# Performance work log

Hardware: AMD Instinct MI355X
Metric: run time of the kernel (lower is better)

The kernel has to match this reference:

```python
import jax, jax.numpy as jnp
import numpy as np

H = 4      # SSM / attn heads (d_model/headdim = 256/64)
WIN = 4    # attention window over bands


def _ln(x, g, b):
    m = jnp.mean(x, -1, keepdims=True)
    v = jnp.mean((x - m) ** 2, -1, keepdims=True)
    return (x - m) * jax.lax.rsqrt(v + 1e-5) * g + b


def setup_inputs() -> dict:
    key = jax.random.key(0)
    ks = jax.random.split(key, 24)
    def rn(i, shape, s=0.05):
        return jax.random.normal(ks[i], shape, jnp.float32) * s
    B, T, K, D = 2, 256, 8, 256
    return {
        "z": rn(0, (B, T, K, D), 1.0),
        "ln1_g": jnp.ones((D,), jnp.float32), "ln1_b": jnp.zeros((D,), jnp.float32),
        "Wx": rn(1, (D, D)), "conv_w": rn(2, (D, 4), 0.3), "Wz": rn(3, (D, D)),
        "Wb": rn(4, (D, H * 128)), "Wc": rn(5, (D, H * 128)), "Wdt": rn(6, (D, H)),
        "dt_bias": rn(7, (H,), 0.5), "A_log": rn(8, (H,), 0.5), "theta": rn(9, (H,), 1.0),
        "D_skip": rn(10, (H,), 1.0), "mimo_U": rn(11, (H, H), 0.5), "mimo_V": rn(12, (H, H), 0.5),
        "Wout": rn(13, (D, D)),
        "ln2_g": jnp.ones((D,), jnp.float32), "ln2_b": jnp.zeros((D,), jnp.float32),
        "attn_in_w": rn(14, (3 * D, D)), "attn_in_b": rn(15, (3 * D,), 0.02),
        "attn_out_w": rn(16, (D, D)), "attn_out_b": jnp.zeros((D,), jnp.float32),
        "ln3_g": jnp.ones((D,), jnp.float32), "ln3_b": jnp.zeros((D,), jnp.float32),
        "Wg": rn(17, (D, 4 * D)), "Wu": rn(18, (D, 4 * D)), "Wd": rn(19, (4 * D, D)),
    }


def _forward(z, ln1_g, ln1_b, Wx, conv_w, Wz, Wb, Wc, Wdt, dt_bias, A_log, theta,
             D_skip, mimo_U, mimo_V, Wout, ln2_g, ln2_b, attn_in_w, attn_in_b,
             attn_out_w, attn_out_b, ln3_g, ln3_b, Wg, Wu, Wd):
    B, T, K, D = z.shape
    P = D // H
    N = Wb.shape[1] // H
    # ---------- (a) intra-band Mamba3 (complex MIMO selective scan) ----------
    u = _ln(z, ln1_g, ln1_b)
    u = jnp.transpose(u, (0, 2, 1, 3)).reshape(B * K, T, D)   # [BK,T,D]
    x = u @ Wx
    # causal depthwise conv1d, kernel 4
    xp = jnp.pad(x, ((0, 0), (3, 0), (0, 0)))
    x = sum(xp[:, k:k + T, :] * conv_w[:, k] for k in range(4))
    x = jax.nn.silu(x)
    xh = x.reshape(B * K, T, H, P)
    Bm = (u @ Wb).reshape(B * K, T, H, N)
    Cm = (u @ Wc).reshape(B * K, T, H, N)
    Mmix = mimo_U @ mimo_V.T                                  # rank-r cross-head coupling
    Bm = jnp.einsum('hg,btgn->bthn', Mmix, Bm)
    dt = jax.nn.softplus(u @ Wdt + dt_bias)                   # [BK,T,H]
    A = -jnp.exp(A_log)                                       # stable real decay
    mag = jnp.exp(dt * A)
    ph = dt * theta                                           # harmonic rotation
    ar, ai = mag * jnp.cos(ph), mag * jnp.sin(ph)
    xs = tuple(jnp.moveaxis(t, 1, 0) for t in (xh, Bm, Cm, dt, ar, ai))
    h0 = jnp.zeros((B * K, H, N, P), x.dtype)

    def step(carry, s):
        h_re, h_im = carry
        xt, bt, ct, dtt, art, ait = s
        dBx = (dtt[:, :, None, None] * bt[:, :, :, None]) * xt[:, :, None, :]
        nr = art[:, :, None, None] * h_re - ait[:, :, None, None] * h_im + dBx
        ni = art[:, :, None, None] * h_im + ait[:, :, None, None] * h_re
        return (nr, ni), jnp.einsum('bhn,bhnp->bhp', ct, nr)   # Re(C . h)

    _, ys = jax.lax.scan(step, (h0, h0), xs)                  # ys: [T,BK,H,P]
    y = jnp.moveaxis(ys, 0, 1) + D_skip[None, None, :, None] * xh
    y = y.reshape(B * K, T, D) * jax.nn.silu(u @ Wz)
    y = y @ Wout
    z = z + jnp.transpose(y.reshape(B, K, T, D), (0, 2, 1, 3))
    # ---------- (b) inter-band windowed attention ----------
    zn = _ln(z, ln2_g, ln2_b).reshape(B * T, K, D)
    qkv = zn @ attn_in_w.T + attn_in_b
    q, k_, v = jnp.split(qkv, 3, axis=-1)
    hd = D // H
    def hs(t):
        return t.reshape(B * T, K // WIN, WIN, H, hd).transpose(0, 1, 3, 2, 4)
    q, k_, v = hs(q), hs(k_), hs(v)
    s = jnp.einsum('mwhqd,mwhkd->mwhqk', q, k_) * jnp.float32(1.0 / np.sqrt(hd))
    a = jax.nn.softmax(s, axis=-1)
    o = jnp.einsum('mwhqk,mwhkd->mwhqd', a, v).transpose(0, 1, 3, 2, 4).reshape(B * T, K, D)
    z = z + (o @ attn_out_w.T + attn_out_b).reshape(B, T, K, D)
    # ---------- (c) SwiGLU FFN ----------
    zf = _ln(z, ln3_g, ln3_b)
    z = z + (jax.nn.silu(zf @ Wg) * (zf @ Wu)) @ Wd
    return z


def reference(z, ln1_g, ln1_b, Wx, conv_w, Wz, Wb, Wc, Wdt, dt_bias, A_log, theta,
              D_skip, mimo_U, mimo_V, Wout, ln2_g, ln2_b, attn_in_w, attn_in_b,
              attn_out_w, attn_out_b, ln3_g, ln3_b, Wg, Wu, Wd):
    return _forward(z, ln1_g, ln1_b, Wx, conv_w, Wz, Wb, Wc, Wdt, dt_bias, A_log,
                    theta, D_skip, mimo_U, mimo_V, Wout, ln2_g, ln2_b, attn_in_w,
                    attn_in_b, attn_out_w, attn_out_b, ln3_g, ln3_b, Wg, Wu, Wd)
```

## Files before the change

kernel.cpp:

```cpp
#include <hip/hip_runtime.h>
#include <hip/hip_bf16.h>
#include <math.h>

typedef __hip_bfloat16 bf16;
typedef __attribute__((ext_vector_type(8))) short s16x8;
typedef __attribute__((ext_vector_type(4))) float f32x4;

__device__ __forceinline__ float siluf(float x) { return x / (1.f + __expf(-x)); }
__device__ __forceinline__ float bits2f(unsigned short u) {
    union { float f; unsigned i; } v; v.i = ((unsigned)u) << 16; return v.f;
}
__device__ __forceinline__ unsigned short f2bits(float f) {
    return (unsigned short)__bfloat16_as_ushort(__float2bfloat16(f));
}

#define KFL 1024
#define OFF_UB   (768*KFL)
#define OFF_DTV  (1280*KFL)
#define OFF_BMB  (1344*KFL)
#define OFF_CMB  (2368*KFL)
#define OFF_ZGB  (3392*KFL)
#define OFF_XB   (3904*KFL)
#define OFF_X2T  (4928*KFL)
#define OFF_P    (5440*KFL)
// ... 66 lines not shown
                for (int j = 0; j < 4; j++) s += U[h * 4 + j] * V[g * 4 + j];
                mm[g] = s;
            }
            #pragma unroll
            for (int i = 0; i < 16; i++) {
                int idx = tid + i * 256;
                int kk = idx >> 6, nn = idx & 63;
                const float* row = src + (size_t)(k0 + kk) * 512 + scol + nn;
                lds[kk * 65 + nn] = mm[0] * row[0] + mm[1] * row[128]
                                  + mm[2] * row[256] + mm[3] * row[384];
            }
        } else {
            #pragma unroll
            for (int i = 0; i < 16; i++) {
                int idx = tid + i * 256;
                int kk = idx >> 6, nn = idx & 63;
                lds[kk * 65 + nn] = src[(size_t)(k0 + kk) * srcN + sc0 + nn];
            }
        }
        __syncthreads();
        #pragma unroll
        for (int i = 0; i < 16; i++) {
            int idx = tid + i * 256;
            int nn = idx >> 6, kk = idx & 63;
            wout[dstoff + (size_t)(n0 + nn) * dstK + k0 + kk] = f2bits(lds[kk * 65 + nn]);
        }
        return;
    }
    int r = blk - 368;
    float* lds = smem;
    float* dts = smem + 4;
    int t = r & 255, bk = r >> 8;
    int b_ = bk >> 3, k = bk & 7;
    int srcr = ((b_ * 256 + t) * 8 + k) * 256;
    int d = tid;
    float x = z[srcr + d];
    float v = x;
    #pragma unroll
    for (int off = 32; off; off >>= 1) v += __shfl_xor(v, off, 64);
    if ((d & 63) == 0) lds[d >> 6] = v;
    __syncthreads();
    float mean = (lds[0] + lds[1] + lds[2] + lds[3]) * (1.f / 256.f);
    __syncthreads();
    float c = x - mean;
    v = c * c;
    #pragma unroll
    for (int off = 32; off; off >>= 1) v += __shfl_xor(v, off, 64);
    if ((d & 63) == 0) lds[d >> 6] = v;
    __syncthreads();
    float var = (lds[0] + lds[1] + lds[2] + lds[3]) * (1.f / 256.f);
    float uval = c * rsqrtf(var + 1e-5f) * g1[d] + b1[d];
    u[r * 256 + d] = f2bits(uval);
    float4 wv = *(const float4*)(Wdt + d * 4);
    float q0 = uval * wv.x, q1 = uval * wv.y, q2 = uval * wv.z, q3 = uval * wv.w;
    #pragma unroll
    for (int off = 32; off; off >>= 1) {
        q0 += __shfl_xor(q0, off, 64);
        q1 += __shfl_xor(q1, off, 64);
        q2 += __shfl_xor(q2, off, 64);
        q3 += __shfl_xor(q3, off, 64);
    }
    if ((d & 63) == 0) {
        int w = d >> 6;
        dts[w * 4 + 0] = q0; dts[w * 4 + 1] = q1;
        dts[w * 4 + 2] = q2; dts[w * 4 + 3] = q3;
    }
    __syncthreads();
    if (d == 0) {
        float dv[4];
        #pragma unroll
        for (int h = 0; h < 4; h++) {
            float xx = dts[h] + dts[4 + h] + dts[8 + h] + dts[12 + h] + dt_bias[h];
            dv[h] = (xx > 20.f) ? xx : log1pf(__expf(xx));
        }
        dtv4[r] = make_float4(dv[0], dv[1], dv[2], dv[3]);
    }
}

__global__ __launch_bounds__(256) void gemm_bczx(
    const unsigned short* __restrict__ A, const unsigned short* __restrict__ Bt,
    unsigned short* __restrict__ bmb, unsigned short* __restrict__ cmb,
    unsigned short* __restrict__ zgb, unsigned short* __restrict__ xb)
{
    __shared__ __align__(16) unsigned short As[128 * 72];
    __shared__ __align__(16) unsigned short Bs[128 * 72];
    const int K = 256;
    int tid = threadIdx.x;
    int n0 = blockIdx.x * 128, m0 = blockIdx.y * 128;
    int w = tid >> 6, l = tid & 63;
    int mwave = (w >> 1) * 64, nwave = (w & 1) * 64;
    f32x4 acc[4][4] = {};
    int srow = tid >> 3, sc = (tid & 7) * 8;
    const unsigned short* Ap = A + (size_t)(m0 + srow) * K + sc;
    const unsigned short* Bp = Bt + (size_t)(n0 + srow) * K + sc;
    int lq = l & 15, lh = l >> 4;
    uint4 a0 = *(const uint4*)(Ap);
    uint4 a1 = *(const uint4*)(Ap + (size_t)32 * K);
    uint4 a2 = *(const uint4*)(Ap + (size_t)64 * K);
    uint4 a3 = *(const uint4*)(Ap + (size_t)96 * K);
    uint4 b0 = *(const uint4*)(Bp);
    uint4 b1 = *(const uint4*)(Bp + (size_t)32 * K);
    uint4 b2 = *(const uint4*)(Bp + (size_t)64 * K);
    uint4 b3 = *(const uint4*)(Bp + (size_t)96 * K);
    for (int k0 = 0; k0 < K; k0 += 64) {
        if (k0) __syncthreads();
        *(uint4*)&As[srow * 72 + sc] = a0;
        *(uint4*)&As[(srow + 32) * 72 + sc] = a1;
        *(uint4*)&As[(srow + 64) * 72 + sc] = a2;
        *(uint4*)&As[(srow + 96) * 72 + sc] = a3;
        *(uint4*)&Bs[srow * 72 + sc] = b0;
        *(uint4*)&Bs[(srow + 32) * 72 + sc] = b1;
        *(uint4*)&Bs[(srow + 64) * 72 + sc] = b2;
        *(uint4*)&Bs[(srow + 96) * 72 + sc] = b3;
        __syncthreads();
        if (k0 + 64 < K) {
            a0 = *(const uint4*)(Ap + k0 + 64);
            a1 = *(const uint4*)(Ap + (size_t)32 * K + k0 + 64);
            a2 = *(const uint4*)(Ap + (size_t)64 * K + k0 + 64);
            a3 = *(const uint4*)(Ap + (size_t)96 * K + k0 + 64);
            b0 = *(const uint4*)(Bp + k0 + 64);
            b1 = *(const uint4*)(Bp + (size_t)32 * K + k0 + 64);
            b2 = *(const uint4*)(Bp + (size_t)64 * K + k0 + 64);
            b3 = *(const uint4*)(Bp + (size_t)96 * K + k0 + 64);
        }
        #pragma unroll
        for (int kk = 0; kk < 2; kk++) {
            int kof = kk * 32 + lh * 8;
            s16x8 bfr[4];
            #pragma unroll
            for (int nf = 0; nf < 4; nf++)
                bfr[nf] = *(const s16x8*)&Bs[(nwave + nf * 16 + lq) * 72 + kof];
            #pragma unroll
            for (int mf = 0; mf < 4; mf++) {
                s16x8 af = *(const s16x8*)&As[(mwave + mf * 16 + lq) * 72 + kof];
                #pragma unroll
                for (int nf = 0; nf < 4; nf++)
                    acc[mf][nf] = __builtin_amdgcn_mfma_f32_16x16x32_bf16(af, bfr[nf], acc[mf][nf], 0, 0, 0);
            }
        }
    }
    #pragma unroll
    for (int mf = 0; mf < 4; mf++) {
        #pragma unroll
        for (int nf = 0; nf < 4; nf++) {
            int n = n0 + nwave + nf * 16 + lq;
            #pragma unroll
            for (int r = 0; r < 4; r++) {
                int m = m0 + mwave + mf * 16 + (l >> 4) * 4 + r;
                float v = acc[mf][nf][r];
                if (n < 512)       bmb[(size_t)m * 512 + n] = f2bits(v);
                else if (n < 1024) cmb[(size_t)m * 512 + (n - 512)] = f2bits(v);
                else if (n < 1280) zgb[(size_t)m * 256 + (n - 1024)] = f2bits(siluf(v));
                else               xb[(size_t)m * 256 + (n - 1280)] = f2bits(v);
            }
        }
    }
}

__global__ __launch_bounds__(256) void s_conv_kernel(
    const unsigned short* __restrict__ cmb, const unsigned short* __restrict__ bmb,
    const float4* __restrict__ dtv4, const float* __restrict__ A_log,
    const float* __restrict__ theta, unsigned short* __restrict__ P,
    const unsigned short* __restrict__ xb, const float* __restrict__ cw,
    unsigned short* __restrict__ x2t)
{
    __shared__ __align__(16) char smem[39936];
    int blk = blockIdx.x;
    int tid = threadIdx.x;
    if (blk >= 192) {
        int c = blk - 192;
        int bhid = c >> 2, tt = c & 3;
        int bk = bhid >> 2, h = bhid & 3;
        int t0 = tt * 64;
        float* tile = (float*)smem;
        #pragma unroll
        for (int i = 0; i < 17; i++) {
            int idx = tid + i * 256;
            if (idx < 67 * 64) {
                int tr = idx >> 6, dd = idx & 63;
                int t = t0 - 3 + tr;
                tile[tr * 65 + dd] = (t >= 0)
                    ? bits2f(xb[(size_t)(bk * 256 + t) * 256 + h * 64 + dd]) : 0.f;
            }
        }
        __syncthreads();
        int wv_ = tid >> 6, lt = tid & 63;
        #pragma unroll 4
        for (int pi = 0; pi < 16; pi++) {
            int p = wv_ * 16 + pi;
            float4 wv = *(const float4*)(cw + (h * 64 + p) * 4);
            float acc = tile[lt * 65 + p] * wv.x + tile[(lt + 1) * 65 + p] * wv.y +
                        tile[(lt + 2) * 65 + p] * wv.z + tile[(lt + 3) * 65 + p] * wv.w;
            x2t[(size_t)(bhid * 64 + p) * 256 + t0 + lt] = f2bits(siluf(acc));
        }
        return;
    }
    int map = blk >> 6;
    int bh = blk & 63;
    int bx = (map == 2) ? 1 : 0;
    int by = (map == 0) ? 0 : 1;
    int bk = bh >> 2, h = bh & 3;
    unsigned short* As = (unsigned short*)smem;
    unsigned short* Bs = As + 128 * 72;
    float* mAs = (float*)(smem + 36864);
    float* phs = mAs + 256;
    float* dss = phs + 256;
    int srow = tid >> 3, sc = (tid & 7) * 8;
    const unsigned short* Ap = cmb + (size_t)(bk * 256 + by * 128 + srow) * 512 + h * 128 + sc;
    const unsigned short* Bp = bmb + (size_t)(bk * 256 + bx * 128 + srow) * 512 + h * 128 + sc;
    uint4 a0 = *(const uint4*)(Ap);
    uint4 a1 = *(const uint4*)(Ap + (size_t)32 * 512);
    uint4 a2 = *(const uint4*)(Ap + (size_t)64 * 512);
    uint4 a3 = *(const uint4*)(Ap + (size_t)96 * 512);
    uint4 b0 = *(const uint4*)(Bp);
    uint4 b1 = *(const uint4*)(Bp + (size_t)32 * 512);
    uint4 b2 = *(const uint4*)(Bp + (size_t)64 * 512);
    uint4 b3 = *(const uint4*)(Bp + (size_t)96 * 512);
    {
        float4 dv = dtv4[bk * 256 + tid];
        float dth = (h == 0) ? dv.x : (h == 1) ? dv.y : (h == 2) ? dv.z : dv.w;
        float Ah = -__expf(A_log[h]);
        float th = theta[h];
        dss[tid] = dth;
        mAs[tid] = dth * Ah;
        phs[tid] = dth * th;
        __syncthreads();
        for (int off = 1; off < 256; off <<= 1) {
            float a = 0.f, p = 0.f;
            int use = (tid >= off);
            if (use) { a = mAs[tid - off]; p = phs[tid - off]; }
            __syncthreads();
            if (use) { mAs[tid] += a; phs[tid] += p; }
            __syncthreads();
        }
    }
    int w = tid >> 6, l = tid & 63;
    int mwave = (w >> 1) * 64, nwave = (w & 1) * 64;
    int lq = l & 15, lh = l >> 4;
    unsigned short* Pout = P + (size_t)bh * 65536;
    f32x4 acc[4][4] = {};
    for (int k0 = 0; k0 < 128; k0 += 64) {
        __syncthreads();
        *(uint4*)&As[srow * 72 + sc] = a0;
        *(uint4*)&As[(srow + 32) * 72 + sc] = a1;
        *(uint4*)&As[(srow + 64) * 72 + sc] = a2;
        *(uint4*)&As[(srow + 96) * 72 + sc] = a3;
        *(uint4*)&Bs[srow * 72 + sc] = b0;
        *(uint4*)&Bs[(srow + 32) * 72 + sc] = b1;
        *(uint4*)&Bs[(srow + 64) * 72 + sc] = b2;
        *(uint4*)&Bs[(srow + 96) * 72 + sc] = b3;
        __syncthreads();
        if (k0 + 64 < 128) {
            a0 = *(const uint4*)(Ap + k0 + 64);
            a1 = *(const uint4*)(Ap + (size_t)32 * 512 + k0 + 64);
            a2 = *(const uint4*)(Ap + (size_t)64 * 512 + k0 + 64);
            a3 = *(const uint4*)(Ap + (size_t)96 * 512 + k0 + 64);
            b0 = *(const uint4*)(Bp + k0 + 64);
            b1 = *(const uint4*)(Bp + (size_t)32 * 512 + k0 + 64);
            b2 = *(const uint4*)(Bp + (size_t)64 * 512 + k0 + 64);
            b3 = *(const uint4*)(Bp + (size_t)96 * 512 + k0 + 64);
        }
        #pragma unroll
        for (int kk = 0; kk < 2; kk++) {
            int kof = kk * 32 + lh * 8;
            s16x8 bfr[4];
            #pragma unroll
            for (int nf = 0; nf < 4; nf++)
                bfr[nf] = *(const s16x8*)&Bs[(nwave + nf * 16 + lq) * 72 + kof];
            #pragma unroll
            for (int mf = 0; mf < 4; mf++) {
                s16x8 af = *(const s16x8*)&As[(mwave + mf * 16 + lq) * 72 + kof];
                #pragma unroll
                for (int nf = 0; nf < 4; nf++)
                    acc[mf][nf] = __builtin_amdgcn_mfma_f32_16x16x32_bf16(af, bfr[nf], acc[mf][nf], 0, 0, 0);
            }
        }
    }
    #pragma unroll
    for (int mf = 0; mf < 4; mf++) {
        float tmv[4], tpv[4]; int tg[4];
        #pragma unroll
        for (int r = 0; r < 4; r++) {
            tg[r] = by * 128 + mwave + mf * 16 + lh * 4 + r;
            tmv[r] = mAs[tg[r]];
            tpv[r] = phs[tg[r]];
        }
        #pragma unroll
        for (int nf = 0; nf < 4; nf++) {
            int s = bx * 128 + nwave + nf * 16 + lq;
            float ms = mAs[s];
            float ps = phs[s];
            float ds = dss[s];
            #pragma unroll
            for (int r = 0; r < 4; r++) {
                float wgt = (s <= tg[r])
                    ? __expf(tmv[r] - ms) * __cosf(tpv[r] - ps) * ds : 0.f;
                Pout[tg[r] * 256 + s] = f2bits(acc[mf][nf][r] * wgt);
            }
        }
    }
}

__global__ __launch_bounds__(256) void gemm_y(
    const unsigned short* __restrict__ P, const unsigned short* __restrict__ x2t,
    const unsigned short* __restrict__ zgb, const float* __restrict__ Dsk,
    unsigned short* __restrict__ ygb)
{
    int by = blockIdx.x, bh = blockIdx.y;
    int bk = bh >> 2, h = bh & 3;
    int tid = threadIdx.x;
    int w = tid >> 6, l = tid & 63;
    int mw = (w >> 1) * 32, nw = (w & 1) * 32;
    int lq = l & 15, lh = l >> 4;
    __shared__ __align__(16) unsigned short As[64 * 72];
    __shared__ __align__(16) unsigned short Bs[64 * 72];
    f32x4 acc[2][2] = {};
    int srow = tid >> 3, sc = (tid & 7) * 8;
    const unsigned short* Ap = P + (size_t)bh * 65536 + (size_t)(by * 64 + srow) * 256 + sc;
    const unsigned short* Bp = x2t + (size_t)bh * 16384 + (size_t)srow * 256 + sc;
    int kmax = (by + 1) * 64; if (kmax > 256) kmax = 256;
    uint4 a0 = *(const uint4*)(Ap);
    uint4 a1 = *(const uint4*)(Ap + (size_t)32 * 256);
    uint4 b0 = *(const uint4*)(Bp);
    uint4 b1 = *(const uint4*)(Bp + (size_t)32 * 256);
    for (int k0 = 0; k0 < kmax; k0 += 64) {
        if (k0) __syncthreads();
        *(uint4*)&As[srow * 72 + sc] = a0;
        *(uint4*)&As[(srow + 32) * 72 + sc] = a1;
        *(uint4*)&Bs[srow * 72 + sc] = b0;
        *(uint4*)&Bs[(srow + 32) * 72 + sc] = b1;
        __syncthreads();
        if (k0 + 64 < kmax) {
            a0 = *(const uint4*)(Ap + k0 + 64);
            a1 = *(const uint4*)(Ap + (size_t)32 * 256 + k0 + 64);
            b0 = *(const uint4*)(Bp + k0 + 64);
            b1 = *(const uint4*)(Bp + (size_t)32 * 256 + k0 + 64);
        }
        #pragma unroll
        for (int kk = 0; kk < 2; kk++) {
            int kof = kk * 32 + lh * 8;
            s16x8 bfr[2];
            #pragma unroll
            for (int nf = 0; nf < 2; nf++)
                bfr[nf] = *(const s16x8*)&Bs[(nw + nf * 16 + lq) * 72 + kof];
            #pragma unroll
            for (int mf = 0; mf < 2; mf++) {
                s16x8 af = *(const s16x8*)&As[(mw + mf * 16 + lq) * 72 + kof];
                #pragma unroll
                for (int nf = 0; nf < 2; nf++)
                    acc[mf][nf] = __builtin_amdgcn_mfma_f32_16x16x32_bf16(af, bfr[nf], acc[mf][nf], 0, 0, 0);
            }
        }
    }
    float dsk = Dsk[h];
    #pragma unroll
    for (int mf = 0; mf < 2; mf++) {
        #pragma unroll
        for (int nf = 0; nf < 2; nf++) {
            int p = nw + nf * 16 + lq;
            #pragma unroll
            for (int r = 0; r < 4; r++) {
                int t = by * 64 + mw + mf * 16 + lh * 4 + r;
                float xv = bits2f(x2t[(size_t)bh * 16384 + p * 256 + t]);
                float zg = bits2f(zgb[(size_t)(bk * 256 + t) * 256 + h * 64 + p]);
                ygb[(size_t)(bk * 256 + t) * 256 + h * 64 + p] =
                    f2bits((acc[mf][nf][r] + dsk * xv) * zg);
            }
        }
    }
}

__global__ __launch_bounds__(256) void mid_kernel(
    const unsigned short* __restrict__ ygb, const unsigned short* __restrict__ wts,
    const float* __restrict__ zin,
    const float* __restrict__ g2, const float* __restrict__ b2,
    const float* __restrict__ qbias, const float* __restrict__ obias,
    const float* __restrict__ g3, const float* __restrict__ b3,
    float* __restrict__ z2, unsigned short* __restrict__ zfb)
{
    __shared__ __align__(16) char smem[64512];
    unsigned short* Bs = (unsigned short*)smem;
    unsigned short* As = (unsigned short*)(smem + 36864);
    unsigned short* zn = (unsigned short*)(smem + 39168);
    float* z1s = (float*)(smem + 47616);
    float (*partS)[4] = (float(*)[4])(smem + 64000);
    float (*partQ)[4] = (float(*)[4])(smem + 64256);
    unsigned short* qk = (unsigned short*)smem;

    const int K = 256;
    int tid = threadIdx.x;
    int m0 = blockIdx.x * 16;
    int w = tid >> 6, l = tid & 63;
    int nw = w * 64;
    int lq = l & 15, lh = l >> 4;
    int srow = tid >> 3, sc = (tid & 7) * 8;

    {
        int rb = m0 + (srow & 15);
        int irow = ((rb >> 11) * 8 + (rb & 7)) * 256 + ((rb >> 3) & 255);
        const unsigned short* Ap = ygb + (size_t)irow * K + sc;
        const unsigned short* Bp = wts + W_OUT + (size_t)srow * K + sc;
        f32x4 acc[4] = {};
        uint4 a0 = *(const uint4*)(Ap);
        uint4 c0 = *(const uint4*)(Bp);
        uint4 c1 = *(const uint4*)(Bp + (size_t)32 * K);
        uint4 c2 = *(const uint4*)(Bp + (size_t)64 * K);
        uint4 c3 = *(const uint4*)(Bp + (size_t)96 * K);
        uint4 c4 = *(const uint4*)(Bp + (size_t)128 * K);
        uint4 c5 = *(const uint4*)(Bp + (size_t)160 * K);
        uint4 c6 = *(const uint4*)(Bp + (size_t)192 * K);
        uint4 c7 = *(const uint4*)(Bp + (size_t)224 * K);
        for (int k0 = 0; k0 < K; k0 += 64) {
            if (k0) __syncthreads();
            if (tid < 128) *(uint4*)&As[srow * 72 + sc] = a0;
            *(uint4*)&Bs[srow * 72 + sc] = c0;
            *(uint4*)&Bs[(srow + 32) * 72 + sc] = c1;
            *(uint4*)&Bs[(srow + 64) * 72 + sc] = c2;
            *(uint4*)&Bs[(srow + 96) * 72 + sc] = c3;
            *(uint4*)&Bs[(srow + 128) * 72 + sc] = c4;
            *(uint4*)&Bs[(srow + 160) * 72 + sc] = c5;
            *(uint4*)&Bs[(srow + 192) * 72 + sc] = c6;
            *(uint4*)&Bs[(srow + 224) * 72 + sc] = c7;
            __syncthreads();
            if (k0 + 64 < K) {
                a0 = *(const uint4*)(Ap + k0 + 64);
                c0 = *(const uint4*)(Bp + k0 + 64);
                c1 = *(const uint4*)(Bp + (size_t)32 * K + k0 + 64);
                c2 = *(const uint4*)(Bp + (size_t)64 * K + k0 + 64);
                c3 = *(const uint4*)(Bp + (size_t)96 * K + k0 + 64);
                c4 = *(const uint4*)(Bp + (size_t)128 * K + k0 + 64);
                c5 = *(const uint4*)(Bp + (size_t)160 * K + k0 + 64);
                c6 = *(const uint4*)(Bp + (size_t)192 * K + k0 + 64);
                c7 = *(const uint4*)(Bp + (size_t)224 * K + k0 + 64);
            }
            #pragma unroll
            for (int kk = 0; kk < 2; kk++) {
                int kof = kk * 32 + lh * 8;
                s16x8 af = *(const s16x8*)&As[lq * 72 + kof];
                #pragma unroll
                for (int nf = 0; nf < 4; nf++) {
                    s16x8 bf = *(const s16x8*)&Bs[(nw + nf * 16 + lq) * 72 + kof];
                    acc[nf] = __builtin_amdgcn_mfma_f32_16x16x32_bf16(af, bf, acc[nf], 0, 0, 0);
                }
            }
        }
        #pragma unroll
        for (int r = 0; r < 4; r++) {
            int row = lh * 4 + r;
            float s = 0.f, q = 0.f;
            #pragma unroll
// ... 148 lines not shown
        for (int k0 = 0; k0 < K; k0 += 64) {
            __syncthreads();
            *(uint4*)&Bs[srow * 72 + sc] = c0;
            *(uint4*)&Bs[(srow + 32) * 72 + sc] = c1;
            *(uint4*)&Bs[(srow + 64) * 72 + sc] = c2;
            *(uint4*)&Bs[(srow + 96) * 72 + sc] = c3;
            *(uint4*)&Bs[(srow + 128) * 72 + sc] = c4;
            *(uint4*)&Bs[(srow + 160) * 72 + sc] = c5;
            *(uint4*)&Bs[(srow + 192) * 72 + sc] = c6;
            *(uint4*)&Bs[(srow + 224) * 72 + sc] = c7;
            __syncthreads();
            if (k0 + 64 < K) {
                c0 = *(const uint4*)(Bp4 + k0 + 64);
                c1 = *(const uint4*)(Bp4 + (size_t)32 * K + k0 + 64);
                c2 = *(const uint4*)(Bp4 + (size_t)64 * K + k0 + 64);
                c3 = *(const uint4*)(Bp4 + (size_t)96 * K + k0 + 64);
                c4 = *(const uint4*)(Bp4 + (size_t)128 * K + k0 + 64);
                c5 = *(const uint4*)(Bp4 + (size_t)160 * K + k0 + 64);
                c6 = *(const uint4*)(Bp4 + (size_t)192 * K + k0 + 64);
                c7 = *(const uint4*)(Bp4 + (size_t)224 * K + k0 + 64);
            }
            #pragma unroll
            for (int kk = 0; kk < 2; kk++) {
                int kof = kk * 32 + lh * 8;
                s16x8 af = *(const s16x8*)&zn[lq * 264 + k0 + kof];
                #pragma unroll
                for (int nf = 0; nf < 4; nf++) {
                    s16x8 bf = *(const s16x8*)&Bs[(nw + nf * 16 + lq) * 72 + kof];
                    ac4[nf] = __builtin_amdgcn_mfma_f32_16x16x32_bf16(af, bf, ac4[nf], 0, 0, 0);
                }
            }
        }
        float bv[4], gv[4], bbv[4];
        #pragma unroll
        for (int nf = 0; nf < 4; nf++) {
            int n = nw + nf * 16 + lq;
            bv[nf] = obias[n];
            gv[nf] = g3[n];
            bbv[nf] = b3[n];
        }
        #pragma unroll
        for (int r = 0; r < 4; r++) {
            int row = lh * 4 + r;
            float s = 0.f, q = 0.f;
            #pragma unroll
            for (int nf = 0; nf < 4; nf++) {
                float v = ac4[nf][r] + bv[nf] + z1s[row * 256 + nw + nf * 16 + lq];
                ac4[nf][r] = v;
                s += v; q += v * v;
            }
            #pragma unroll
            for (int off = 1; off < 16; off <<= 1) {
                s += __shfl_xor(s, off, 64);
                q += __shfl_xor(q, off, 64);
            }
            if (lq == 0) { partS[row][w] = s; partQ[row][w] = q; }
        }
        __syncthreads();
        #pragma unroll
        for (int r = 0; r < 4; r++) {
            int row = lh * 4 + r;
            float sum = partS[row][0] + partS[row][1] + partS[row][2] + partS[row][3];
            float sq  = partQ[row][0] + partQ[row][1] + partQ[row][2] + partQ[row][3];
            float mean = sum * (1.f / 256.f);
            float var = sq * (1.f / 256.f) - mean * mean;
            float rstd = rsqrtf(var + 1e-5f);
            size_t ro = (size_t)(m0 + row) * 256;
            #pragma unroll
            for (int nf = 0; nf < 4; nf++) {
                int n = nw + nf * 16 + lq;
                float v = ac4[nf][r];
                z2[ro + n] = v;
                zfb[ro + n] = f2bits((v - mean) * rstd * gv[nf] + bbv[nf]);
            }
        }
    }
}

__global__ __launch_bounds__(256) void gemm_gu2(
    const unsigned short* __restrict__ A, const unsigned short* __restrict__ Wgu,
    unsigned short* __restrict__ gg)
{
    const int K = 256;
    __shared__ __align__(16) unsigned short As[128 * 72];
    __shared__ __align__(16) unsigned short Bgs[64 * 72];
    __shared__ __align__(16) unsigned short Bus[64 * 72];
    int tid = threadIdx.x;
    int n0 = blockIdx.x * 64, m0 = blockIdx.y * 128;
    int w = tid >> 6, l = tid & 63;
    int mwave = (w >> 1) * 64, nwave = (w & 1) * 32;
    int lq = l & 15, lh = l >> 4;
    f32x4 ag[4][2] = {}, au[4][2] = {};
    int srow = tid >> 3, sc = (tid & 7) * 8;
    const unsigned short* Ap = A + (size_t)(m0 + srow) * K + sc;
    const unsigned short* Bgp = Wgu + (size_t)(n0 + srow) * K + sc;
    const unsigned short* Bup = Wgu + (size_t)(1024 + n0 + srow) * K + sc;
    uint4 a0 = *(const uint4*)(Ap);
    uint4 a1 = *(const uint4*)(Ap + (size_t)32 * K);
    uint4 a2 = *(const uint4*)(Ap + (size_t)64 * K);
    uint4 a3 = *(const uint4*)(Ap + (size_t)96 * K);
    uint4 bg0 = *(const uint4*)(Bgp);
    uint4 bg1 = *(const uint4*)(Bgp + (size_t)32 * K);
    uint4 bu0 = *(const uint4*)(Bup);
    uint4 bu1 = *(const uint4*)(Bup + (size_t)32 * K);
    for (int k0 = 0; k0 < K; k0 += 64) {
        if (k0) __syncthreads();
        *(uint4*)&As[srow * 72 + sc] = a0;
        *(uint4*)&As[(srow + 32) * 72 + sc] = a1;
        *(uint4*)&As[(srow + 64) * 72 + sc] = a2;
        *(uint4*)&As[(srow + 96) * 72 + sc] = a3;
        *(uint4*)&Bgs[srow * 72 + sc] = bg0;
        *(uint4*)&Bgs[(srow + 32) * 72 + sc] = bg1;
        *(uint4*)&Bus[srow * 72 + sc] = bu0;
        *(uint4*)&Bus[(srow + 32) * 72 + sc] = bu1;
        __syncthreads();
        if (k0 + 64 < K) {
            a0 = *(const uint4*)(Ap + k0 + 64);
            a1 = *(const uint4*)(Ap + (size_t)32 * K + k0 + 64);
            a2 = *(const uint4*)(Ap + (size_t)64 * K + k0 + 64);
            a3 = *(const uint4*)(Ap + (size_t)96 * K + k0 + 64);
            bg0 = *(const uint4*)(Bgp + k0 + 64);
            bg1 = *(const uint4*)(Bgp + (size_t)32 * K + k0 + 64);
            bu0 = *(const uint4*)(Bup + k0 + 64);
            bu1 = *(const uint4*)(Bup + (size_t)32 * K + k0 + 64);
        }
        #pragma unroll
        for (int kk = 0; kk < 2; kk++) {
            int kof = kk * 32 + lh * 8;
            s16x8 bgr[2], bur[2];
            #pragma unroll
            for (int nf = 0; nf < 2; nf++) {
                bgr[nf] = *(const s16x8*)&Bgs[(nwave + nf * 16 + lq) * 72 + kof];
                bur[nf] = *(const s16x8*)&Bus[(nwave + nf * 16 + lq) * 72 + kof];
            }
            #pragma unroll
            for (int mf = 0; mf < 4; mf++) {
                s16x8 af = *(const s16x8*)&As[(mwave + mf * 16 + lq) * 72 + kof];
                #pragma unroll
                for (int nf = 0; nf < 2; nf++) {
                    ag[mf][nf] = __builtin_amdgcn_mfma_f32_16x16x32_bf16(af, bgr[nf], ag[mf][nf], 0, 0, 0);
                    au[mf][nf] = __builtin_amdgcn_mfma_f32_16x16x32_bf16(af, bur[nf], au[mf][nf], 0, 0, 0);
                }
            }
        }
    }
    #pragma unroll
    for (int mf = 0; mf < 4; mf++) {
        #pragma unroll
        for (int nf = 0; nf < 2; nf++) {
            int n = n0 + nwave + nf * 16 + lq;
            #pragma unroll
            for (int r = 0; r < 4; r++) {
                int m = m0 + mwave + mf * 16 + lh * 4 + r;
                gg[(size_t)m * 1024 + n] = f2bits(siluf(ag[mf][nf][r]) * au[mf][nf][r]);
            }
        }
    }
}

__global__ __launch_bounds__(256) void gemm_d2(
    const unsigned short* __restrict__ gg, const unsigned short* __restrict__ Bt,
    const float* __restrict__ resid, float* __restrict__ out)
{
    __shared__ __align__(16) unsigned short As[64 * 72];
    __shared__ __align__(16) unsigned short Bs[64 * 72];
    const int K = 1024, N = 256;
    int tid = threadIdx.x;
    int n0 = blockIdx.x * 64, m0 = blockIdx.y * 64;
    int w = tid >> 6, l = tid & 63;
    int mw = (w >> 1) * 32, nw = (w & 1) * 32;
    f32x4 acc[2][2] = {};
    int srow = tid >> 3, sc = (tid & 7) * 8;
    const unsigned short* Ap = gg + (size_t)(m0 + srow) * K + sc;
    const unsigned short* Bp = Bt + (size_t)(n0 + srow) * K + sc;
    int lq = l & 15, lh = l >> 4;
    uint4 a0 = *(const uint4*)(Ap);
    uint4 a1 = *(const uint4*)(Ap + (size_t)32 * K);
    uint4 b0 = *(const uint4*)(Bp);
    uint4 b1 = *(const uint4*)(Bp + (size_t)32 * K);
    for (int k0 = 0; k0 < K; k0 += 64) {
        if (k0) __syncthreads();
        *(uint4*)&As[srow * 72 + sc] = a0;
        *(uint4*)&As[(srow + 32) * 72 + sc] = a1;
        *(uint4*)&Bs[srow * 72 + sc] = b0;
        *(uint4*)&Bs[(srow + 32) * 72 + sc] = b1;
        __syncthreads();
        if (k0 + 64 < K) {
            a0 = *(const uint4*)(Ap + k0 + 64);
            a1 = *(const uint4*)(Ap + (size_t)32 * K + k0 + 64);
            b0 = *(const uint4*)(Bp + k0 + 64);
            b1 = *(const uint4*)(Bp + (size_t)32 * K + k0 + 64);
        }
        #pragma unroll
        for (int kk = 0; kk < 2; kk++) {
            int kof = kk * 32 + lh * 8;
            s16x8 bfr[2];
            #pragma unroll
            for (int nf = 0; nf < 2; nf++)
                bfr[nf] = *(const s16x8*)&Bs[(nw + nf * 16 + lq) * 72 + kof];
            #pragma unroll
            for (int mf = 0; mf < 2; mf++) {
                s16x8 af = *(const s16x8*)&As[(mw + mf * 16 + lq) * 72 + kof];
                #pragma unroll
                for (int nf = 0; nf < 2; nf++)
                    acc[mf][nf] = __builtin_amdgcn_mfma_f32_16x16x32_bf16(af, bfr[nf], acc[mf][nf], 0, 0, 0);
            }
        }
    }
    #pragma unroll
    for (int mf = 0; mf < 2; mf++) {
        #pragma unroll
        for (int nf = 0; nf < 2; nf++) {
            int n = n0 + nw + nf * 16 + lq;
            #pragma unroll
            for (int r = 0; r < 4; r++) {
                int m = m0 + mw + mf * 16 + lh * 4 + r;
                out[(size_t)m * N + n] = acc[mf][nf][r] + resid[(size_t)m * N + n];
            }
        }
    }
}

extern "C" void kernel_launch(void* const* d_in, const int* in_sizes, int n_in,
                              void* d_out, int out_size, void* d_ws, size_t ws_size,
                              hipStream_t stream)
{
    const float* z         = (const float*)d_in[0];
    const float* ln1_g     = (const float*)d_in[1];
    const float* ln1_b     = (const float*)d_in[2];
    const float* Wx        = (const float*)d_in[3];
    const float* conv_w    = (const float*)d_in[4];
    const float* Wz        = (const float*)d_in[5];
    const float* Wb        = (const float*)d_in[6];
    const float* Wc        = (const float*)d_in[7];
    const float* Wdt       = (const float*)d_in[8];
    const float* dt_bias   = (const float*)d_in[9];
    const float* A_log     = (const float*)d_in[10];
    const float* theta     = (const float*)d_in[11];
    const float* D_skip    = (const float*)d_in[12];
    const float* mimo_U    = (const float*)d_in[13];
    const float* mimo_V    = (const float*)d_in[14];
    const float* Wout      = (const float*)d_in[15];
    const float* ln2_g     = (const float*)d_in[16];
    const float* ln2_b     = (const float*)d_in[17];
    const float* attn_in_w = (const float*)d_in[18];
    const float* attn_in_b = (const float*)d_in[19];
    const float* attn_out_w= (const float*)d_in[20];
    const float* attn_out_b= (const float*)d_in[21];
    const float* ln3_g     = (const float*)d_in[22];
    const float* ln3_b     = (const float*)d_in[23];
    const float* Wg        = (const float*)d_in[24];
    const float* Wu        = (const float*)d_in[25];
    const float* Wd        = (const float*)d_in[26];

    float* W = (float*)d_ws;
    unsigned short* wts = (unsigned short*)W;
    unsigned short* ub  = (unsigned short*)(W + OFF_UB);
    float4* dtv4        = (float4*)(W + OFF_DTV);
    unsigned short* bmb = (unsigned short*)(W + OFF_BMB);
    unsigned short* cmb = (unsigned short*)(W + OFF_CMB);
    unsigned short* zgb = (unsigned short*)(W + OFF_ZGB);
    unsigned short* xb  = (unsigned short*)(W + OFF_XB);
    unsigned short* x2t = (unsigned short*)(W + OFF_X2T);
    unsigned short* pbuf= (unsigned short*)(W + OFF_P);
    unsigned short* ygb = (unsigned short*)(W + OFF_YGB);
    float* z2           = W + OFF_Z2;
    unsigned short* zfb = (unsigned short*)(W + OFF_ZFB);
    unsigned short* gg  = (unsigned short*)(W + OFF_GG);

    prep_ln1_kernel<<<4464, 256, 0, stream>>>(
        Wx, Wb, Wc, Wz, Wout, attn_in_w, attn_out_w, Wg, Wu, Wd, mimo_U, mimo_V,
        wts, z, ln1_g, ln1_b, Wdt, dt_bias, ub, dtv4);
    gemm_bczx<<<dim3(12, 32), 256, 0, stream>>>(ub, wts + W_BCZX, bmb, cmb, zgb, xb);
    s_conv_kernel<<<448, 256, 0, stream>>>(cmb, bmb, dtv4, A_log, theta, pbuf,
                                           xb, conv_w, x2t);
    gemm_y<<<dim3(4, 64), 256, 0, stream>>>(pbuf, x2t, zgb, D_skip, ygb);
    mid_kernel<<<256, 256, 0, stream>>>(ygb, wts, z, ln2_g, ln2_b,
                                        attn_in_b, attn_out_b, ln3_g, ln3_b,
                                        z2, zfb);
    gemm_gu2<<<dim3(16, 32), 256, 0, stream>>>(zfb, wts + W_GU, gg);
    gemm_d2<<<dim3(4, 64), 256, 0, stream>>>(gg, wts + W_D, z2, (float*)d_out);
}
```

Before: 198.6 us.

## Halve GEMM tiles to double grid sizes and use wave-shuffle prefix scan

Halves the M or N tile size in the four GEMM kernels (bczx, y, gu2, d2) and doubles their grid dimensions, so more workgroups are spread across the many compute units. The intent is to fill the GPU better on these small problems. The cost is less data reuse per tile and more redundant loads of the shared operand. Separately, the 256-element prefix scan in s_conv is replaced: a shared-memory Hillis-Steele loop with many barriers becomes a per-wave __shfl_up scan plus a cross-wave offset step. This removes most __syncthreads calls. In gemm_y the causal k-limit is recomputed for 32-row tiles.

New measurement: 198.7 us. Within noise of the previous version (+0.1%).

```diff
diff --git a/kernel.cpp b/kernel.cpp
--- a/kernel.cpp
+++ b/kernel.cpp
@@ -172,22 +172,20 @@
     unsigned short* __restrict__ bmb, unsigned short* __restrict__ cmb,
     unsigned short* __restrict__ zgb, unsigned short* __restrict__ xb)
 {
-    __shared__ __align__(16) unsigned short As[128 * 72];
+    __shared__ __align__(16) unsigned short As[64 * 72];
     __shared__ __align__(16) unsigned short Bs[128 * 72];
     const int K = 256;
     int tid = threadIdx.x;
-    int n0 = blockIdx.x * 128, m0 = blockIdx.y * 128;
+    int n0 = blockIdx.x * 128, m0 = blockIdx.y * 64;
     int w = tid >> 6, l = tid & 63;
-    int mwave = (w >> 1) * 64, nwave = (w & 1) * 64;
-    f32x4 acc[4][4] = {};
+    int mwave = (w >> 1) * 32, nwave = (w & 1) * 64;
+    f32x4 acc[2][4] = {};
     int srow = tid >> 3, sc = (tid & 7) * 8;
     const unsigned short* Ap = A + (size_t)(m0 + srow) * K + sc;
     const unsigned short* Bp = Bt + (size_t)(n0 + srow) * K + sc;
     int lq = l & 15, lh = l >> 4;
     uint4 a0 = *(const uint4*)(Ap);
     uint4 a1 = *(const uint4*)(Ap + (size_t)32 * K);
-    uint4 a2 = *(const uint4*)(Ap + (size_t)64 * K);
-    uint4 a3 = *(const uint4*)(Ap + (size_t)96 * K);
     uint4 b0 = *(const uint4*)(Bp);
     uint4 b1 = *(const uint4*)(Bp + (size_t)32 * K);
     uint4 b2 = *(const uint4*)(Bp + (size_t)64 * K);
@@ -196,8 +194,6 @@
         if (k0) __syncthreads();
         *(uint4*)&As[srow * 72 + sc] = a0;
         *(uint4*)&As[(srow + 32) * 72 + sc] = a1;
-        *(uint4*)&As[(srow + 64) * 72 + sc] = a2;
-        *(uint4*)&As[(srow + 96) * 72 + sc] = a3;
         *(uint4*)&Bs[srow * 72 + sc] = b0;
         *(uint4*)&Bs[(srow + 32) * 72 + sc] = b1;
         *(uint4*)&Bs[(srow + 64) * 72 + sc] = b2;
@@ -206,8 +202,6 @@
         if (k0 + 64 < K) {
             a0 = *(const uint4*)(Ap + k0 + 64);
             a1 = *(const uint4*)(Ap + (size_t)32 * K + k0 + 64);
-            a2 = *(const uint4*)(Ap + (size_t)64 * K + k0 + 64);
-            a3 = *(const uint4*)(Ap + (size_t)96 * K + k0 + 64);
             b0 = *(const uint4*)(Bp + k0 + 64);
             b1 = *(const uint4*)(Bp + (size_t)32 * K + k0 + 64);
             b2 = *(const uint4*)(Bp + (size_t)64 * K + k0 + 64);
@@ -221,7 +215,7 @@
             for (int nf = 0; nf < 4; nf++)
                 bfr[nf] = *(const s16x8*)&Bs[(nwave + nf * 16 + lq) * 72 + kof];
             #pragma unroll
-            for (int mf = 0; mf < 4; mf++) {
+            for (int mf = 0; mf < 2; mf++) {
                 s16x8 af = *(const s16x8*)&As[(mwave + mf * 16 + lq) * 72 + kof];
                 #pragma unroll
                 for (int nf = 0; nf < 4; nf++)
@@ -230,13 +224,13 @@
         }
     }
     #pragma unroll
-    for (int mf = 0; mf < 4; mf++) {
+    for (int mf = 0; mf < 2; mf++) {
         #pragma unroll
         for (int nf = 0; nf < 4; nf++) {
             int n = n0 + nwave + nf * 16 + lq;
             #pragma unroll
             for (int r = 0; r < 4; r++) {
-                int m = m0 + mwave + mf * 16 + (l >> 4) * 4 + r;
+                int m = m0 + mwave + mf * 16 + lh * 4 + r;
                 float v = acc[mf][nf][r];
                 if (n < 512)       bmb[(size_t)m * 512 + n] = f2bits(v);
                 else if (n < 1024) cmb[(size_t)m * 512 + (n - 512)] = f2bits(v);
@@ -311,18 +305,25 @@
         float dth = (h == 0) ? dv.x : (h == 1) ? dv.y : (h == 2) ? dv.z : dv.w;
         float Ah = -__expf(A_log[h]);
         float th = theta[h];
+        float a = dth * Ah, p = dth * th;
         dss[tid] = dth;
-        mAs[tid] = dth * Ah;
-        phs[tid] = dth * th;
-        __syncthreads();
-        for (int off = 1; off < 256; off <<= 1) {
-            float a = 0.f, p = 0.f;
-            int use = (tid >= off);
-            if (use) { a = mAs[tid - off]; p = phs[tid - off]; }
-            __syncthreads();
-            if (use) { mAs[tid] += a; phs[tid] += p; }
-            __syncthreads();
-        }
+        int lane = tid & 63, wv = tid >> 6;
+        #pragma unroll
+        for (int off = 1; off < 64; off <<= 1) {
+            float ta = __shfl_up(a, off, 64);
+            float tp = __shfl_up(p, off, 64);
+            if (lane >= off) { a += ta; p += tp; }
+        }
+        if (lane == 63) { mAs[wv] = a; phs[wv] = p; }
+        __syncthreads();
+        float offA = 0.f, offP = 0.f;
+        #pragma unroll
+        for (int j = 0; j < 3; j++)
+            if (j < wv) { offA += mAs[j]; offP += phs[j]; }
+        __syncthreads();
+        mAs[tid] = a + offA;
+        phs[tid] = p + offP;
+        __syncthreads();
     }
     int w = tid >> 6, l = tid & 63;
     int mwave = (w >> 1) * 64, nwave = (w & 1) * 64;
@@ -398,64 +399,56 @@
 {
     int by = blockIdx.x, bh = blockIdx.y;
     int bk = bh >> 2, h = bh & 3;
+    int t0 = by * 32;
     int tid = threadIdx.x;
     int w = tid >> 6, l = tid & 63;
-    int mw = (w >> 1) * 32, nw = (w & 1) * 32;
+    int mw = (w >> 1) * 16, nw = (w & 1) * 32;
     int lq = l & 15, lh = l >> 4;
-    __shared__ __align__(16) unsigned short As[64 * 72];
+    __shared__ __align__(16) unsigned short As[32 * 72];
     __shared__ __align__(16) unsigned short Bs[64 * 72];
-    f32x4 acc[2][2] = {};
+    f32x4 acc[2] = {};
     int srow = tid >> 3, sc = (tid & 7) * 8;
-    const unsigned short* Ap = P + (size_t)bh * 65536 + (size_t)(by * 64 + srow) * 256 + sc;
+    const unsigned short* Ap = P + (size_t)bh * 65536 + (size_t)(t0 + srow) * 256 + sc;
     const unsigned short* Bp = x2t + (size_t)bh * 16384 + (size_t)srow * 256 + sc;
-    int kmax = (by + 1) * 64; if (kmax > 256) kmax = 256;
+    int kmax = ((by >> 1) + 1) * 64;
     uint4 a0 = *(const uint4*)(Ap);
-    uint4 a1 = *(const uint4*)(Ap + (size_t)32 * 256);
     uint4 b0 = *(const uint4*)(Bp);
     uint4 b1 = *(const uint4*)(Bp + (size_t)32 * 256);
     for (int k0 = 0; k0 < kmax; k0 += 64) {
         if (k0) __syncthreads();
-        *(uint4*)&As[srow * 72 + sc] = a0;
-        *(uint4*)&As[(srow + 32) * 72 + sc] = a1;
+        if (tid < 256) {
+            *(uint4*)&As[(srow & 31) * 72 + sc] = a0;
+        }
         *(uint4*)&Bs[srow * 72 + sc] = b0;
         *(uint4*)&Bs[(srow + 32) * 72 + sc] = b1;
         __syncthreads();
         if (k0 + 64 < kmax) {
             a0 = *(const uint4*)(Ap + k0 + 64);
-            a1 = *(const uint4*)(Ap + (size_t)32 * 256 + k0 + 64);
             b0 = *(const uint4*)(Bp + k0 + 64);
             b1 = *(const uint4*)(Bp + (size_t)32 * 256 + k0 + 64);
         }
         #pragma unroll
         for (int kk = 0; kk < 2; kk++) {
             int kof = kk * 32 + lh * 8;
-            s16x8 bfr[2];
-            #pragma unroll
-            for (int nf = 0; nf < 2; nf++)
-                bfr[nf] = *(const s16x8*)&Bs[(nw + nf * 16 + lq) * 72 + kof];
-            #pragma unroll
-            for (int mf = 0; mf < 2; mf++) {
-                s16x8 af = *(const s16x8*)&As[(mw + mf * 16 + lq) * 72 + kof];
-                #pragma unroll
-                for (int nf = 0; nf < 2; nf++)
-                    acc[mf][nf] = __builtin_amdgcn_mfma_f32_16x16x32_bf16(af, bfr[nf], acc[mf][nf], 0, 0, 0);
+            s16x8 af = *(const s16x8*)&As[(mw + lq) * 72 + kof];
+            #pragma unroll
+            for (int nf = 0; nf < 2; nf++) {
+                s16x8 bf = *(const s16x8*)&Bs[(nw + nf * 16 + lq) * 72 + kof];
+                acc[nf] = __builtin_amdgcn_mfma_f32_16x16x32_bf16(af, bf, acc[nf], 0, 0, 0);
             }
         }
     }
     float dsk = Dsk[h];
     #pragma unroll
-    for (int mf = 0; mf < 2; mf++) {
-        #pragma unroll
-        for (int nf = 0; nf < 2; nf++) {
-            int p = nw + nf * 16 + lq;
-            #pragma unroll
-            for (int r = 0; r < 4; r++) {
-                int t = by * 64 + mw + mf * 16 + lh * 4 + r;
-                float xv = bits2f(x2t[(size_t)bh * 16384 + p * 256 + t]);
-                float zg = bits2f(zgb[(size_t)(bk * 256 + t) * 256 + h * 64 + p]);
-                ygb[(size_t)(bk * 256 + t) * 256 + h * 64 + p] =
-                    f2bits((acc[mf][nf][r] + dsk * xv) * zg);
-            }
+    for (int nf = 0; nf < 2; nf++) {
+        int p = nw + nf * 16 + lq;
+        #pragma unroll
+        for (int r = 0; r < 4; r++) {
+            int t = t0 + mw + lh * 4 + r;
+            float xv = bits2f(x2t[(size_t)bh * 16384 + p * 256 + t]);
+            float zg = bits2f(zgb[(size_t)(bk * 256 + t) * 256 + h * 64 + p]);
+            ygb[(size_t)(bk * 256 + t) * 256 + h * 64 + p] =
+                f2bits((acc[nf][r] + dsk * xv) * zg);
         }
     }
 }
@@ -770,23 +763,21 @@
     unsigned short* __restrict__ gg)
 {
     const int K = 256;
-    __shared__ __align__(16) unsigned short As[128 * 72];
+    __shared__ __align__(16) unsigned short As[64 * 72];
     __shared__ __align__(16) unsigned short Bgs[64 * 72];
     __shared__ __align__(16) unsigned short Bus[64 * 72];
     int tid = threadIdx.x;
-    int n0 = blockIdx.x * 64, m0 = blockIdx.y * 128;
+    int n0 = blockIdx.x * 64, m0 = blockIdx.y * 64;
     int w = tid >> 6, l = tid & 63;
-    int mwave = (w >> 1) * 64, nwave = (w & 1) * 32;
+    int mwave = (w >> 1) * 32, nwave = (w & 1) * 32;
     int lq = l & 15, lh = l >> 4;
-    f32x4 ag[4][2] = {}, au[4][2] = {};
+    f32x4 ag[2][2] = {}, au[2][2] = {};
     int srow = tid >> 3, sc = (tid & 7) * 8;
     const unsigned short* Ap = A + (size_t)(m0 + srow) * K + sc;
     const unsigned short* Bgp = Wgu + (size_t)(n0 + srow) * K + sc;
     const unsigned short* Bup = Wgu + (size_t)(1024 + n0 + srow) * K + sc;
     uint4 a0 = *(const uint4*)(Ap);
     uint4 a1 = *(const uint4*)(Ap + (size_t)32 * K);
-    uint4 a2 = *(const uint4*)(Ap + (size_t)64 * K);
-    uint4 a3 = *(const uint4*)(Ap + (size_t)96 * K);
     uint4 bg0 = *(const uint4*)(Bgp);
     uint4 bg1 = *(const uint4*)(Bgp + (size_t)32 * K);
     uint4 bu0 = *(const uint4*)(Bup);
@@ -795,8 +786,6 @@
         if (k0) __syncthreads();
         *(uint4*)&As[srow * 72 + sc] = a0;
         *(uint4*)&As[(srow + 32) * 72 + sc] = a1;
-        *(uint4*)&As[(srow + 64) * 72 + sc] = a2;
-        *(uint4*)&As[(srow + 96) * 72 + sc] = a3;
         *(uint4*)&Bgs[srow * 72 + sc] = bg0;
         *(uint4*)&Bgs[(srow + 32) * 72 + sc] = bg1;
         *(uint4*)&Bus[srow * 72 + sc] = bu0;
@@ -805,8 +794,6 @@
         if (k0 + 64 < K) {
             a0 = *(const uint4*)(Ap + k0 + 64);
             a1 = *(const uint4*)(Ap + (size_t)32 * K + k0 + 64);
-            a2 = *(const uint4*)(Ap + (size_t)64 * K + k0 + 64);
-            a3 = *(const uint4*)(Ap + (size_t)96 * K + k0 + 64);
             bg0 = *(const uint4*)(Bgp + k0 + 64);
             bg1 = *(const uint4*)(Bgp + (size_t)32 * K + k0 + 64);
             bu0 = *(const uint4*)(Bup + k0 + 64);
@@ -822,7 +809,7 @@
                 bur[nf] = *(const s16x8*)&Bus[(nwave + nf * 16 + lq) * 72 + kof];
             }
             #pragma unroll
-            for (int mf = 0; mf < 4; mf++) {
+            for (int mf = 0; mf < 2; mf++) {
                 s16x8 af = *(const s16x8*)&As[(mwave + mf * 16 + lq) * 72 + kof];
                 #pragma unroll
                 for (int nf = 0; nf < 2; nf++) {
@@ -833,7 +820,7 @@
         }
     }
     #pragma unroll
-    for (int mf = 0; mf < 4; mf++) {
+    for (int mf = 0; mf < 2; mf++) {
         #pragma unroll
         for (int nf = 0; nf < 2; nf++) {
             int n = n0 + nwave + nf * 16 + lq;
@@ -851,60 +838,49 @@
     const float* __restrict__ resid, float* __restrict__ out)
 {
     __shared__ __align__(16) unsigned short As[64 * 72];
-    __shared__ __align__(16) unsigned short Bs[64 * 72];
+    __shared__ __align__(16) unsigned short Bs[32 * 72];
     const int K = 1024, N = 256;
     int tid = threadIdx.x;
-    int n0 = blockIdx.x * 64, m0 = blockIdx.y * 64;
+    int n0 = blockIdx.x * 32, m0 = blockIdx.y * 64;
     int w = tid >> 6, l = tid & 63;
-    int mw = (w >> 1) * 32, nw = (w & 1) * 32;
-    f32x4 acc[2][2] = {};
+    int mw = (w >> 1) * 32, nw = (w & 1) * 16;
+    f32x4 acc[2] = {};
     int srow = tid >> 3, sc = (tid & 7) * 8;
     const unsigned short* Ap = gg + (size_t)(m0 + srow) * K + sc;
-    const unsigned short* Bp = Bt + (size_t)(n0 + srow) * K + sc;
+    const unsigned short* Bp = Bt + (size_t)(n0 + (srow & 31)) * K + sc;
     int lq = l & 15, lh = l >> 4;
     uint4 a0 = *(const uint4*)(Ap);
     uint4 a1 = *(const uint4*)(Ap + (size_t)32 * K);
     uint4 b0 = *(const uint4*)(Bp);
-    uint4 b1 = *(const uint4*)(Bp + (size_t)32 * K);
     for (int k0 = 0; k0 < K; k0 += 64) {
         if (k0) __syncthreads();
         *(uint4*)&As[srow * 72 + sc] = a0;
         *(uint4*)&As[(srow + 32) * 72 + sc] = a1;
-        *(uint4*)&Bs[srow * 72 + sc] = b0;
-        *(uint4*)&Bs[(srow + 32) * 72 + sc] = b1;
+        if (tid < 256) *(uint4*)&Bs[(srow & 31) * 72 + sc] = b0;
         __syncthreads();
         if (k0 + 64 < K) {
             a0 = *(const uint4*)(Ap + k0 + 64);
             a1 = *(const uint4*)(Ap + (size_t)32 * K + k0 + 64);
             b0 = *(const uint4*)(Bp + k0 + 64);
-            b1 = *(const uint4*)(Bp + (size_t)32 * K + k0 + 64);
         }
         #pragma unroll
         for (int kk = 0; kk < 2; kk++) {
             int kof = kk * 32 + lh * 8;
-            s16x8 bfr[2];
-            #pragma unroll
-            for (int nf = 0; nf < 2; nf++)
-                bfr[nf] = *(const s16x8*)&Bs[(nw + nf * 16 + lq) * 72 + kof];
+            s16x8 bf = *(const s16x8*)&Bs[(nw + lq) * 72 + kof];
             #pragma unroll
             for (int mf = 0; mf < 2; mf++) {
                 s16x8 af = *(const s16x8*)&As[(mw + mf * 16 + lq) * 72 + kof];
-                #pragma unroll
-                for (int nf = 0; nf < 2; nf++)
-                    acc[mf][nf] = __builtin_amdgcn_mfma_f32_16x16x32_bf16(af, bfr[nf], acc[mf][nf], 0, 0, 0);
-            }
-        }
-    }
+                acc[mf] = __builtin_amdgcn_mfma_f32_16x16x32_bf16(af, bf, acc[mf], 0, 0, 0);
+            }
+        }
+    }
+    int n = n0 + nw + lq;
     #pragma unroll
     for (int mf = 0; mf < 2; mf++) {
         #pragma unroll
-        for (int nf = 0; nf < 2; nf++) {
-            int n = n0 + nw + nf * 16 + lq;
-            #pragma unroll
-            for (int r = 0; r < 4; r++) {
-                int m = m0 + mw + mf * 16 + lh * 4 + r;
-                out[(size_t)m * N + n] = acc[mf][nf][r] + resid[(size_t)m * N + n];
-            }
+        for (int r = 0; r < 4; r++) {
+            int m = m0 + mw + mf * 16 + lh * 4 + r;
+            out[(size_t)m * N + n] = acc[mf][r] + resid[(size_t)m * N + n];
         }
     }
 }
@@ -959,13 +935,13 @@
     prep_ln1_kernel<<<4464, 256, 0, stream>>>(
         Wx, Wb, Wc, Wz, Wout, attn_in_w, attn_out_w, Wg, Wu, Wd, mimo_U, mimo_V,
         wts, z, ln1_g, ln1_b, Wdt, dt_bias, ub, dtv4);
-    gemm_bczx<<<dim3(12, 32), 256, 0, stream>>>(ub, wts + W_BCZX, bmb, cmb, zgb, xb);
+    gemm_bczx<<<dim3(12, 64), 256, 0, stream>>>(ub, wts + W_BCZX, bmb, cmb, zgb, xb);
     s_conv_kernel<<<448, 256, 0, stream>>>(cmb, bmb, dtv4, A_log, theta, pbuf,
                                            xb, conv_w, x2t);
-    gemm_y<<<dim3(4, 64), 256, 0, stream>>>(pbuf, x2t, zgb, D_skip, ygb);
+    gemm_y<<<dim3(8, 64), 256, 0, stream>>>(pbuf, x2t, zgb, D_skip, ygb);
     mid_kernel<<<256, 256, 0, stream>>>(ygb, wts, z, ln2_g, ln2_b,
                                         attn_in_b, attn_out_b, ln3_g, ln3_b,
                                         z2, zfb);
-    gemm_gu2<<<dim3(16, 32), 256, 0, stream>>>(zfb, wts + W_GU, gg);
-    gemm_d2<<<dim3(4, 64), 256, 0, stream>>>(gg, wts + W_D, z2, (float*)d_out);
+    gemm_gu2<<<dim3(16, 64), 256, 0, stream>>>(zfb, wts + W_GU, gg);
+    gemm_d2<<<dim3(8, 64), 256, 0, stream>>>(gg, wts + W_D, z2, (float*)d_out);
 }
```
